# Optimization experiments

Measured on AMD Instinct MI355X. Metric: run time of the kernel, lower is better.

The kernel has to match this reference:

```python
import math
import jax, jax.numpy as jnp
import numpy as np

FACIL_RATE = 2.0
FIRE_THRESH = 0.85
MAX_GATE = 8.0
EPS = 1e-12  # F.normalize eps

B, T, D = 8, 4096, 2048


def _gelu(x):
    # tanh-approx GELU, exactly as in the torch module
    c = math.sqrt(2.0 / math.pi)
    return 0.5 * x * (1.0 + jnp.tanh(c * (x + 0.044715 * x * x * x)))


def _l2norm(v, axis=-1):
    n = jnp.sqrt(jnp.sum(v * v, axis=axis, keepdims=True))
    return v / jnp.maximum(n, EPS)


def setup_inputs() -> dict:
    key = jax.random.key(0)
    k1, k2 = jax.random.split(key)
    x = jax.random.normal(k1, (B, T, D), dtype=jnp.float32)
    pos_buf = jax.random.normal(k2, (T, D), dtype=jnp.float32)
    pos_facil = jnp.ones((T,), dtype=jnp.float32)
    log_k_pos = jnp.asarray(math.log(0.5), dtype=jnp.float32)
    return {"x": x, "log_k_pos": log_k_pos, "pos_buf": pos_buf, "pos_facil": pos_facil}


def reference(x, log_k_pos, pos_buf, pos_facil):
    # steady-state (pass1 complete) path of GELU275.forward
    k_pos = jnp.clip(jnp.exp(log_k_pos), 0.01, 5.0)
    y = _gelu(x)                                   # [B,T,D]
    # everything below the gelu except the final gate multiply runs under
    # no_grad / on y.detach() in torch -> stop_gradient here
    y_det = jax.lax.stop_gradient(y)
    pos_buf_n = _l2norm(jax.lax.stop_gradient(pos_buf))          # [T,D]
    y_n = _l2norm(y_det)                                          # [B,T,D]
    sim = jnp.einsum("btd,td->bt", y_n, pos_buf_n)               # cosine sim [B,T]
    fire_mask = jnp.mean(sim, axis=0) > FIRE_THRESH              # [T]
    pf = jax.lax.stop_gradient(pos_facil)
    facil_t = jnp.where(fire_mask, jnp.minimum(pf * FACIL_RATE, 16.0), pf)  # [T]
    gate = jnp.minimum(1.0 + k_pos * (facil_t[None, :] - 1.0) * sim, MAX_GATE)  # [B,T]
    return y * gate[:, :, None]
```

## Files before the change

### kernel.cpp

```cpp
#include <hip/hip_runtime.h>
#include <math.h>

#define BB 8
#define TT 4096
#define DD 2048
#define THREADS 512
#define NWAVES (THREADS / 64)

__device__ __forceinline__ float fast_tanh(float a) {
    float e = __expf(2.0f * a);
    return 1.0f - 2.0f / (e + 1.0f);
}

__device__ __forceinline__ float gelu_tanh(float x) {
    const float c = 0.7978845608028654f;
    float inner = c * (x + 0.044715f * x * x * x);
    return 0.5f * x * (1.0f + fast_tanh(inner));
}

__global__ __launch_bounds__(THREADS) void gelu275_fused(
    const float* __restrict__ x,
    const float* __restrict__ log_k_pos,
    const float* __restrict__ pos_buf,
    const float* __restrict__ pos_facil,
    float* __restrict__ out)
{
    const int t    = blockIdx.x;
    const int tid  = threadIdx.x;
    const int lane = tid & 63;
    const int wave = tid >> 6;

    __shared__ float red[NWAVES * 17];
    __shared__ float s_gate[BB];

    const float4 p4 = *reinterpret_cast<const float4*>(
        pos_buf + (size_t)t * DD + (size_t)tid * 4);
    const float pp[4] = {p4.x, p4.y, p4.z, p4.w};
    float pn2 = pp[0]*pp[0] + pp[1]*pp[1] + pp[2]*pp[2] + pp[3]*pp[3];

    float y[BB][4];
    float dotp[BB];
    float yn2[BB];
#pragma unroll
    for (int b = 0; b < BB; ++b) {
        const float4 x4 = *reinterpret_cast<const float4*>(
            x + ((size_t)b * TT + t) * DD + (size_t)tid * 4);
        const float xs[4] = {x4.x, x4.y, x4.z, x4.w};
        float d = 0.0f, n = 0.0f;
#pragma unroll
        for (int j = 0; j < 4; ++j) {
            float yv = gelu_tanh(xs[j]);
            y[b][j] = yv;
            d += yv * pp[j];
            n += yv * yv;
        }
        dotp[b] = d;
        yn2[b]  = n;
    }

#pragma unroll
    for (int off = 32; off; off >>= 1) {
        pn2 += __shfl_xor(pn2, off);
#pragma unroll
        for (int b = 0; b < BB; ++b) {
            dotp[b] += __shfl_xor(dotp[b], off);
            yn2[b]  += __shfl_xor(yn2[b],  off);
        }
    }
    if (lane == 0) {
        red[wave * 17 + 0] = pn2;
#pragma unroll
        for (int b = 0; b < BB; ++b) {
            red[wave * 17 + 1 + b] = dotp[b];
            red[wave * 17 + 9 + b] = yn2[b];
        }
    }
    __syncthreads();

    if (tid == 0) {
        float P = 0.0f;
        float Dt[BB], Yn[BB];
#pragma unroll
        for (int b = 0; b < BB; ++b) { Dt[b] = 0.0f; Yn[b] = 0.0f; }
        for (int w = 0; w < NWAVES; ++w) {
            P += red[w * 17 + 0];
#pragma unroll
            for (int b = 0; b < BB; ++b) {
                Dt[b] += red[w * 17 + 1 + b];
                Yn[b] += red[w * 17 + 9 + b];
            }
        }
        const float kp = fminf(fmaxf(expf(log_k_pos[0]), 0.01f), 5.0f);
        const float pnorm = fmaxf(sqrtf(P), 1e-12f);

        float sim[BB];
        float simsum = 0.0f;
#pragma unroll
        for (int b = 0; b < BB; ++b) {
            float ynorm = fmaxf(sqrtf(Yn[b]), 1e-12f);
            sim[b] = Dt[b] / (ynorm * pnorm);
            simsum += sim[b];
        }
        const bool  fire  = (simsum * (1.0f / BB)) > 0.85f;
        const float pf    = pos_facil[t];
        const float facil = fire ? fminf(pf * 2.0f, 16.0f) : pf;
#pragma unroll
        for (int b = 0; b < BB; ++b) {
            s_gate[b] = fminf(1.0f + kp * (facil - 1.0f) * sim[b], 8.0f);
        }
    }
    __syncthreads();

#pragma unroll
    for (int b = 0; b < BB; ++b) {
        const float g = s_gate[b];
        float4 o;
        o.x = y[b][0] * g;
        o.y = y[b][1] * g;
        o.z = y[b][2] * g;
        o.w = y[b][3] * g;
        *reinterpret_cast<float4*>(
            out + ((size_t)b * TT + t) * DD + (size_t)tid * 4) = o;
    }
}

extern "C" void kernel_launch(void* const* d_in, const int* in_sizes, int n_in,
                              void* d_out, int out_size, void* d_ws, size_t ws_size,
                              hipStream_t stream) {
    const float* x          = (const float*)d_in[0];
    const float* log_k_pos  = (const float*)d_in[1];
    const float* pos_buf    = (const float*)d_in[2];
    const float* pos_facil  = (const float*)d_in[3];
    float* out              = (float*)d_out;

    dim3 grid(TT);
    dim3 block(THREADS);
    gelu275_fused<<<grid, block, 0, stream>>>(x, log_k_pos, pos_buf, pos_facil, out);
}
```

Before: 129.6 us.

## Halve block size, double per-thread work, shuffle-based gate, nontemporal stores

Cuts the block to 256 threads so each thread processes 8 columns per batch row, and issues all x loads before any compute to raise memory-level parallelism. The serial single-thread gate computation and its second __syncthreads are replaced by a per-lane reduction over the 8 batches with shuffle broadcast. Output is written with nontemporal stores so it does not pollute the cache. The larger per-thread register footprint (64 floats held for x) may limit occupancy, which the launch-bounds hint of 4 tries to keep up.

```diff
diff --git a/kernel.cpp b/kernel.cpp
--- a/kernel.cpp
+++ b/kernel.cpp
@@ -4,8 +4,10 @@
 #define BB 8
 #define TT 4096
 #define DD 2048
-#define THREADS 512
+#define THREADS 256
 #define NWAVES (THREADS / 64)
+
+typedef float v4f __attribute__((ext_vector_type(4)));
 
 __device__ __forceinline__ float fast_tanh(float a) {
     float e = __expf(2.0f * a);
@@ -18,7 +20,15 @@
     return 0.5f * x * (1.0f + fast_tanh(inner));
 }
 
-__global__ __launch_bounds__(THREADS) void gelu275_fused(
+__device__ __forceinline__ void gelu4_dot(v4f& v, const v4f& p,
+                                          float& d, float& n) {
+    v.x = gelu_tanh(v.x); v.y = gelu_tanh(v.y);
+    v.z = gelu_tanh(v.z); v.w = gelu_tanh(v.w);
+    d += v.x * p.x + v.y * p.y + v.z * p.z + v.w * p.w;
+    n += v.x * v.x + v.y * v.y + v.z * v.z + v.w * v.w;
+}
+
+__global__ __launch_bounds__(THREADS, 4) void gelu275_fused(
     const float* __restrict__ x,
     const float* __restrict__ log_k_pos,
     const float* __restrict__ pos_buf,
@@ -30,30 +40,30 @@
     const int lane = tid & 63;
     const int wave = tid >> 6;
 
-    __shared__ float red[NWAVES * 17];
-    __shared__ float s_gate[BB];
+    __shared__ float red[NWAVES][17];
 
-    const float4 p4 = *reinterpret_cast<const float4*>(
-        pos_buf + (size_t)t * DD + (size_t)tid * 4);
-    const float pp[4] = {p4.x, p4.y, p4.z, p4.w};
-    float pn2 = pp[0]*pp[0] + pp[1]*pp[1] + pp[2]*pp[2] + pp[3]*pp[3];
+    const size_t col = (size_t)tid * 8;
 
-    float y[BB][4];
-    float dotp[BB];
-    float yn2[BB];
+    v4f xa[BB], xb[BB];
 #pragma unroll
     for (int b = 0; b < BB; ++b) {
-        const float4 x4 = *reinterpret_cast<const float4*>(
-            x + ((size_t)b * TT + t) * DD + (size_t)tid * 4);
-        const float xs[4] = {x4.x, x4.y, x4.z, x4.w};
+        const float* px = x + ((size_t)b * TT + t) * DD + col;
+        xa[b] = *reinterpret_cast<const v4f*>(px);
+        xb[b] = *reinterpret_cast<const v4f*>(px + 4);
+    }
+    const float* pp = pos_buf + (size_t)t * DD + col;
+    const v4f pa = *reinterpret_cast<const v4f*>(pp);
+    const v4f pb = *reinterpret_cast<const v4f*>(pp + 4);
+
+    float pn2 = pa.x*pa.x + pa.y*pa.y + pa.z*pa.z + pa.w*pa.w
+              + pb.x*pb.x + pb.y*pb.y + pb.z*pb.z + pb.w*pb.w;
+
+    float dotp[BB], yn2[BB];
+#pragma unroll
+    for (int b = 0; b < BB; ++b) {
         float d = 0.0f, n = 0.0f;
-#pragma unroll
-        for (int j = 0; j < 4; ++j) {
-            float yv = gelu_tanh(xs[j]);
-            y[b][j] = yv;
-            d += yv * pp[j];
-            n += yv * yv;
-        }
+        gelu4_dot(xa[b], pa, d, n);
+        gelu4_dot(xb[b], pb, d, n);
         dotp[b] = d;
         yn2[b]  = n;
     }
@@ -68,59 +78,49 @@
         }
     }
     if (lane == 0) {
-        red[wave * 17 + 0] = pn2;
+        red[wave][0] = pn2;
 #pragma unroll
         for (int b = 0; b < BB; ++b) {
-            red[wave * 17 + 1 + b] = dotp[b];
-            red[wave * 17 + 9 + b] = yn2[b];
+            red[wave][1 + b] = dotp[b];
+            red[wave][9 + b] = yn2[b];
         }
     }
     __syncthreads();
 
-    if (tid == 0) {
-        float P = 0.0f;
-        float Dt[BB], Yn[BB];
+    const int myb = lane & 7;
+    float P = 0.0f, Dt = 0.0f, Yn = 0.0f;
 #pragma unroll
-        for (int b = 0; b < BB; ++b) { Dt[b] = 0.0f; Yn[b] = 0.0f; }
-        for (int w = 0; w < NWAVES; ++w) {
-            P += red[w * 17 + 0];
-#pragma unroll
-            for (int b = 0; b < BB; ++b) {
-                Dt[b] += red[w * 17 + 1 + b];
-                Yn[b] += red[w * 17 + 9 + b];
-            }
-        }
-        const float kp = fminf(fmaxf(expf(log_k_pos[0]), 0.01f), 5.0f);
-        const float pnorm = fmaxf(sqrtf(P), 1e-12f);
+    for (int w = 0; w < NWAVES; ++w) {
+        P  += red[w][0];
+        Dt += red[w][1 + myb];
+        Yn += red[w][9 + myb];
+    }
+    const float kp = fminf(fmaxf(__expf(log_k_pos[0]), 0.01f), 5.0f);
+    const float pn = fmaxf(sqrtf(P),  1e-12f);
+    const float yn = fmaxf(sqrtf(Yn), 1e-12f);
+    const float sim = Dt / (yn * pn);
 
-        float sim[BB];
-        float simsum = 0.0f;
-#pragma unroll
-        for (int b = 0; b < BB; ++b) {
-            float ynorm = fmaxf(sqrtf(Yn[b]), 1e-12f);
-            sim[b] = Dt[b] / (ynorm * pnorm);
-            simsum += sim[b];
-        }
-        const bool  fire  = (simsum * (1.0f / BB)) > 0.85f;
-        const float pf    = pos_facil[t];
-        const float facil = fire ? fminf(pf * 2.0f, 16.0f) : pf;
-#pragma unroll
-        for (int b = 0; b < BB; ++b) {
-            s_gate[b] = fminf(1.0f + kp * (facil - 1.0f) * sim[b], 8.0f);
-        }
-    }
-    __syncthreads();
+    float simsum = sim;
+    simsum += __shfl_xor(simsum, 1);
+    simsum += __shfl_xor(simsum, 2);
+    simsum += __shfl_xor(simsum, 4);
+
+    const bool  fire  = (simsum * (1.0f / BB)) > 0.85f;
+    const float pf    = pos_facil[t];
+    const float facil = fire ? fminf(pf * 2.0f, 16.0f) : pf;
+    const float myg   = fminf(1.0f + kp * (facil - 1.0f) * sim, 8.0f);
 
 #pragma unroll
     for (int b = 0; b < BB; ++b) {
-        const float g = s_gate[b];
-        float4 o;
-        o.x = y[b][0] * g;
-        o.y = y[b][1] * g;
-        o.z = y[b][2] * g;
-        o.w = y[b][3] * g;
-        *reinterpret_cast<float4*>(
-            out + ((size_t)b * TT + t) * DD + (size_t)tid * 4) = o;
+        const float g = __shfl(myg, b, 8);
+        float* po = out + ((size_t)b * TT + t) * DD + col;
+        v4f o0, o1;
+        o0.x = xa[b].x * g; o0.y = xa[b].y * g;
+        o0.z = xa[b].z * g; o0.w = xa[b].w * g;
+        o1.x = xb[b].x * g; o1.y = xb[b].y * g;
+        o1.z = xb[b].z * g; o1.w = xb[b].w * g;
+        __builtin_nontemporal_store(o0, reinterpret_cast<v4f*>(po));
+        __builtin_nontemporal_store(o1, reinterpret_cast<v4f*>(po + 4));
     }
 }
 
```

Result: no change. 130.7 us (+0.8%).
